# Optimization experiments

Measured on AMD Instinct MI355X. Metric: run time of the kernel, lower is better.

## Reference

```python
import jax, jax.numpy as jnp
import numpy as np

N_NODES = 30000
N_EDGES = 480000
NODE_DIM = 16
NUM_RADIAL = 8
NUM_ELEMENTS = 120
R_MAX = 5.0
NUM_BLOCKS = 2
N_PATHS = 5  # h0*sh0->0e, h0*sh1->1o, h0*sh2->2e, h1.sh1->0e, h2.sh2->0e


def _sh_basis(u):
    # real spherical harmonics up to l=2, component normalization, on unit vectors u [E,3]
    x, y, z = u[:, 0], u[:, 1], u[:, 2]
    s15 = jnp.sqrt(jnp.asarray(15.0, u.dtype))
    s5 = jnp.sqrt(jnp.asarray(5.0, u.dtype))
    sh1 = jnp.sqrt(jnp.asarray(3.0, u.dtype)) * u                      # [E,3]
    sh2 = jnp.stack([s15 * x * y, s15 * y * z,
                     0.5 * s5 * (3.0 * z * z - 1.0),
                     s15 * x * z, 0.5 * s15 * (x * x - y * y)], -1)    # [E,5]
    return sh1, sh2


def _energy(pos, emb, W_init, Wr, br, W_out, W_read, W1, b1, W2, b2, z, edge_index):
    N = pos.shape[0]
    row, col = edge_index[0], edge_index[1]
    edge_vec = pos[row] - pos[col]                                     # [E,3] gather
    r = jnp.sqrt(jnp.sum(edge_vec * edge_vec, -1) + 1e-12)             # [E]
    n = jnp.arange(1, NUM_RADIAL + 1, dtype=pos.dtype)
    # Bessel radial basis: sqrt(2/rc) * sin(n*pi*r/rc)/r
    radial = jnp.sqrt(2.0 / R_MAX) * jnp.sin(n[None, :] * jnp.pi * r[:, None] / R_MAX) / r[:, None]  # [E,R]
    u = edge_vec / r[:, None]
    sh1, sh2 = _sh_basis(u)

    # initial projection: embedding scalars -> 0e channels; l=1,l=2 start at zero
    h0 = emb[z] @ W_init                                               # [N,C]
    h1 = jnp.zeros((N, NODE_DIM, 3), pos.dtype)
    h2 = jnp.zeros((N, NODE_DIM, 5), pos.dtype)

    for b in range(NUM_BLOCKS):
        w = (radial @ Wr[b] + br[b]).reshape(-1, N_PATHS, NODE_DIM)    # [E,P,C] radial path weights
        h0c, h1c, h2c = h0[col], h1[col], h2[col]
        # scalar messages: h0*sh0 + <h1,sh1> + <h2,sh2>
        m0 = (w[:, 0] * h0c
              + w[:, 3] * jnp.einsum('ecm,em->ec', h1c, sh1)
              + w[:, 4] * jnp.einsum('ecm,em->ec', h2c, sh2))          # [E,C]
        m1 = (w[:, 1] * h0c)[:, :, None] * sh1[:, None, :]             # [E,C,3]
        m2 = (w[:, 2] * h0c)[:, :, None] * sh2[:, None, :]             # [E,C,5]
        a0 = jax.ops.segment_sum(m0, row, num_segments=N)
        a1 = jax.ops.segment_sum(m1, row, num_segments=N)
        a2 = jax.ops.segment_sum(m2, row, num_segments=N)
        h0 = h0 + a0 @ W_out[b, 0]
        h1 = h1 + jnp.einsum('ncm,cd->ndm', a1, W_out[b, 1])
        h2 = h2 + jnp.einsum('ncm,cd->ndm', a2, W_out[b, 2])

    inv = h0 @ W_read                                                  # readout 0e part
    site = jax.nn.silu(inv @ W1 + b1) @ W2 + b2                        # [N,1]
    return jnp.sum(site)


def setup_inputs() -> dict:
    key = jax.random.key(0)
    ks = jax.random.split(key, 12)
    C, R = NODE_DIM, NUM_RADIAL
    s = 1.0 / np.sqrt(C)
    return {
        'pos': jax.random.normal(ks[0], (N_NODES, 3), jnp.float32) * 3.0,
        'z': jax.random.randint(ks[1], (N_NODES,), 0, NUM_ELEMENTS),
        'edge_index': jax.random.randint(ks[2], (2, N_EDGES), 0, N_NODES),
        'emb': jax.random.normal(ks[3], (NUM_ELEMENTS, C), jnp.float32),
        'W_init': jax.random.normal(ks[4], (C, C), jnp.float32) * s,
        'Wr': jax.random.normal(ks[5], (NUM_BLOCKS, R, N_PATHS * C), jnp.float32) / np.sqrt(R),
        'br': jnp.zeros((NUM_BLOCKS, N_PATHS * C), jnp.float32),
        'W_out': jax.random.normal(ks[6], (NUM_BLOCKS, 3, C, C), jnp.float32) * s,
        'W_read': jax.random.normal(ks[7], (C, C), jnp.float32) * s,
        'W1': jax.random.normal(ks[8], (C, C), jnp.float32) * s,
        'b1': jnp.zeros((C,), jnp.float32),
        'W2': jax.random.normal(ks[9], (C, 1), jnp.float32) * s,
        'b2': jnp.zeros((1,), jnp.float32),
    }


def reference(pos, z, edge_index, emb, W_init, Wr, br, W_out, W_read, W1, b1, W2, b2):
    e_fn = lambda p: _energy(p, emb, W_init, Wr, br, W_out, W_read, W1, b1, W2, b2, z, edge_index)
    total, dE_dpos = jax.value_and_grad(e_fn)(pos)
    energy = jnp.reshape(total, (1, 1))
    forces = -dE_dpos
    return energy, forces
```

## Files before the change

### kernel.cpp

```cpp
#include <hip/hip_runtime.h>
#include <math.h>

#ifndef M_PI
#define M_PI 3.14159265358979323846
#endif

static inline int cdiv(int a, int b){ return (a + b - 1) / b; }

#define SQRT3f  1.7320508075688772f
#define SQRT5f  2.23606797749979f
#define SQRT15f 3.872983346207417f
#define KRADf   0.6324555320336759f
#define PI5f    0.6283185307179586f

__device__ __forceinline__ float grp16_sum(float v){
  v += __shfl_xor(v, 1, 64);
  v += __shfl_xor(v, 2, 64);
  v += __shfl_xor(v, 4, 64);
  v += __shfl_xor(v, 8, 64);
  return v;
}

__device__ __forceinline__ void sh_from_u(float ux, float uy, float uz,
                                          float* sh1, float* sh2)
{
  sh1[0] = SQRT3f*ux; sh1[1] = SQRT3f*uy; sh1[2] = SQRT3f*uz;
  sh2[0] = SQRT15f*ux*uy;
  sh2[1] = SQRT15f*uy*uz;
  sh2[2] = 0.5f*SQRT5f*(3.f*uz*uz - 1.f);
  sh2[3] = SQRT15f*ux*uz;
  sh2[4] = 0.5f*SQRT15f*(ux*ux - uy*uy);
}

__global__ void k_hist(const int* __restrict__ ei, int E,
                       int* __restrict__ deg_row, int* __restrict__ deg_col)
{
  int e = blockIdx.x * blockDim.x + threadIdx.x;
  if (e >= E) return;
  atomicAdd(&deg_row[ei[e]], 1);
  atomicAdd(&deg_col[ei[E + e]], 1);
}

__global__ void k_alloc(const int* __restrict__ deg_row, const int* __restrict__ deg_col,
                        int* __restrict__ start_row, int* __restrict__ cur_row,
                        int* __restrict__ start_col, int* __restrict__ cur_col,
                        int* __restrict__ cursors, int N)
{
  int idx = blockIdx.x * blockDim.x + threadIdx.x;
  int lane = threadIdx.x & 63;
  #pragma unroll
  for (int which = 0; which < 2; which++) {
    const int* deg = which ? deg_col : deg_row;
    int* start = which ? start_col : start_row;
    int* cur   = which ? cur_col   : cur_row;
    int v = (idx < N) ? deg[idx] : 0;
    int incl = v;
    #pragma unroll
    for (int d = 1; d < 64; d <<= 1) {
      int y = __shfl_up(incl, d, 64);
      if (lane >= d) incl += y;
    }
    int wtot = __shfl(incl, 63, 64);
    int base = 0;
    if (lane == 63) base = atomicAdd(&cursors[which], wtot);
    base = __shfl(base, 63, 64);
    if (idx < N) { int st = base + incl - v; start[idx] = st; cur[idx] = st; }
  }
}

__global__ void k_scatter_geom(const float* __restrict__ pos, const int* __restrict__ ei, int E,
                               int* __restrict__ cur_row, int* __restrict__ cur_col,
                               float4* __restrict__ geoR,
                               int* __restrict__ colR, int* __restrict__ cposR,
                               int* __restrict__ rowC, int* __restrict__ rposC)
{
  int e = blockIdx.x * blockDim.x + threadIdx.x;
  if (e >= E) return;
  int row = ei[e], col = ei[E + e];
  int pr = atomicAdd(&cur_row[row], 1);
  int pc = atomicAdd(&cur_col[col], 1);
  colR[pr] = col; cposR[pr] = pc;
  rowC[pc] = row; rposC[pc] = pr;

  float px = pos[row*3+0] - pos[col*3+0];
  float py = pos[row*3+1] - pos[col*3+1];
  float pz = pos[row*3+2] - pos[col*3+2];
  float r2 = px*px + py*py + pz*pz + 1e-12f;
  float r = sqrtf(r2);
  float inv_r = 1.0f / r;
  float ux = px*inv_r, uy = py*inv_r, uz = pz*inv_r;
  float x = r * PI5f;
  float s1, c1;
  sincosf(x, &s1, &c1);
  float tc = 2.f * c1;
  float sprev = 0.f, s = s1, cprev = 1.f, cc = c1;
  float Ki = KRADf * inv_r;
  float rad[8], draddr[8];
  const float KPI5 = KRADf * PI5f;
  #pragma unroll
  for (int k = 0; k < 8; k++) {
    rad[k] = Ki * s;
    draddr[k] = (KPI5 * (float)(k+1) * cc - rad[k]) * inv_r;
    float sn = tc*s - sprev; sprev = s; s = sn;
    float cn = tc*cc - cprev; cprev = cc; cc = cn;
  }
  geoR[pr*5+0] = make_float4(rad[0], rad[1], rad[2], rad[3]);
  geoR[pr*5+1] = make_float4(rad[4], rad[5], rad[6], rad[7]);
  geoR[pr*5+2] = make_float4(draddr[0], draddr[1], draddr[2], draddr[3]);
  geoR[pr*5+3] = make_float4(draddr[4], draddr[5], draddr[6], draddr[7]);
  geoR[pr*5+4] = make_float4(ux, uy, uz, inv_r);
}

__global__ void k_node_init(const float* __restrict__ emb, const int* __restrict__ z,
                            const float* __restrict__ W_init, float* __restrict__ h0, int N)
{
  __shared__ float sW[256];
  if (threadIdx.x < 256) sW[threadIdx.x] = W_init[threadIdx.x];
  __syncthreads();
  int n = blockIdx.x * blockDim.x + threadIdx.x;
  if (n >= N) return;
  const float* e = emb + z[n]*16;
  float ev[16];
  #pragma unroll
  for (int k = 0; k < 16; k++) ev[k] = e[k];
  #pragma unroll
  for (int c = 0; c < 16; c++) {
    float s = 0.f;
    #pragma unroll
    for (int k = 0; k < 16; k++) s += ev[k] * sW[k*16+c];
    h0[n*16+c] = s;
  }
}

__global__ void k_fwd_b0(const float* __restrict__ Wr, const float* __restrict__ br,
                         const float* __restrict__ h0_in, const float4* __restrict__ geoR,
                         const int* __restrict__ colR,
                         const int* __restrict__ start_row, const int* __restrict__ deg_row,
                         float* __restrict__ a0, float* __restrict__ a1, float* __restrict__ a2,
                         int N)
{
  int n = blockIdx.x * (blockDim.x >> 4) + (threadIdx.x >> 4);
  int c = threadIdx.x & 15;
  if (n >= N) return;
  float wr0[8], wr1[8], wr2[8];
  #pragma unroll
  for (int k = 0; k < 8; k++) {
    wr0[k] = Wr[k*80 + c];
    wr1[k] = Wr[k*80 + 16 + c];
    wr2[k] = Wr[k*80 + 32 + c];
  }
  float b0v = br[c], b1v = br[16 + c], b2v = br[32 + c];

  float acc0 = 0.f, acc1[3] = {0.f,0.f,0.f}, acc2[5] = {0.f,0.f,0.f,0.f,0.f};

  int i0 = start_row[n], i1 = i0 + deg_row[n];
  float4 G0n = {0,0,0,0}, G1n = {0,0,0,0}, G4n = {0,0,0,0};
  float h0n = 0.f;
  if (i0 < i1) {
    G0n = geoR[i0*5+0]; G1n = geoR[i0*5+1]; G4n = geoR[i0*5+4];
    h0n = h0_in[colR[i0]*16 + c];
  }
  for (int i = i0; i < i1; i++) {
    float4 G0 = G0n, G1 = G1n, G4 = G4n;
    float h0c = h0n;
    if (i+1 < i1) {
      G0n = geoR[(i+1)*5+0]; G1n = geoR[(i+1)*5+1]; G4n = geoR[(i+1)*5+4];
      h0n = h0_in[colR[i+1]*16 + c];
    }
    float rad[8] = {G0.x,G0.y,G0.z,G0.w,G1.x,G1.y,G1.z,G1.w};
    float sh1[3], sh2[5];
    sh_from_u(G4.x, G4.y, G4.z, sh1, sh2);
    float w0 = b0v, w1 = b1v, w2 = b2v;
    #pragma unroll
    for (int k = 0; k < 8; k++) {
      w0 += rad[k]*wr0[k]; w1 += rad[k]*wr1[k]; w2 += rad[k]*wr2[k];
    }
    acc0 += w0*h0c;
    float wh1 = w1*h0c, wh2 = w2*h0c;
    #pragma unroll
    for (int m = 0; m < 3; m++) acc1[m] += wh1*sh1[m];
    #pragma unroll
    for (int m = 0; m < 5; m++) acc2[m] += wh2*sh2[m];
  }
  a0[n*16 + c] = acc0;
  #pragma unroll
  for (int m = 0; m < 3; m++) a1[n*48 + c*3 + m] = acc1[m];
  #pragma unroll
  for (int m = 0; m < 5; m++) a2[n*80 + c*5 + m] = acc2[m];
}

__global__ void k_fwd_b1(const float* __restrict__ Wr, const float* __restrict__ br,
                         const float* __restrict__ h0_in, const float* __restrict__ h1_in,
                         const float* __restrict__ h2_in, const float4* __restrict__ geoR,
                         const int* __restrict__ colR,
                         const int* __restrict__ start_row, const int* __restrict__ deg_row,
                         float* __restrict__ a0, int N)
{
  int n = blockIdx.x * (blockDim.x >> 4) + (threadIdx.x >> 4);
  int c = threadIdx.x & 15;
  if (n >= N) return;
  float wr0[8], wr3[8], wr4[8];
  #pragma unroll
  for (int k = 0; k < 8; k++) {
    wr0[k] = Wr[k*80 + c];
    wr3[k] = Wr[k*80 + 48 + c];
    wr4[k] = Wr[k*80 + 64 + c];
  }
  float b0v = br[c], b3v = br[48 + c], b4v = br[64 + c];

  float acc0 = 0.f;
  int i0 = start_row[n], i1 = i0 + deg_row[n];
  float4 G0n = {0,0,0,0}, G1n = {0,0,0,0}, G4n = {0,0,0,0};
  float h0n = 0.f, h1n[3] = {0,0,0}, h2n[5] = {0,0,0,0,0};
  if (i0 < i1) {
    int col = colR[i0];
    G0n = geoR[i0*5+0]; G1n = geoR[i0*5+1]; G4n = geoR[i0*5+4];
    h0n = h0_in[col*16 + c];
    #pragma unroll
    for (int m = 0; m < 3; m++) h1n[m] = h1_in[col*48 + c*3 + m];
    #pragma unroll
    for (int m = 0; m < 5; m++) h2n[m] = h2_in[col*80 + c*5 + m];
  }
  for (int i = i0; i < i1; i++) {
    float4 G0 = G0n, G1 = G1n, G4 = G4n;
    float h0c = h0n;
    float h1c[3], h2c[5];
    #pragma unroll
    for (int m = 0; m < 3; m++) h1c[m] = h1n[m];
    #pragma unroll
    for (int m = 0; m < 5; m++) h2c[m] = h2n[m];
    if (i+1 < i1) {
      int col = colR[i+1];
      G0n = geoR[(i+1)*5+0]; G1n = geoR[(i+1)*5+1]; G4n = geoR[(i+1)*5+4];
      h0n = h0_in[col*16 + c];
      #pragma unroll
      for (int m = 0; m < 3; m++) h1n[m] = h1_in[col*48 + c*3 + m];
      #pragma unroll
      for (int m = 0; m < 5; m++) h2n[m] = h2_in[col*80 + c*5 + m];
    }
    float rad[8] = {G0.x,G0.y,G0.z,G0.w,G1.x,G1.y,G1.z,G1.w};
    float sh1[3], sh2[5];
    sh_from_u(G4.x, G4.y, G4.z, sh1, sh2);
    float w0 = b0v, w3 = b3v, w4 = b4v;
    #pragma unroll
    for (int k = 0; k < 8; k++) {
      w0 += rad[k]*wr0[k]; w3 += rad[k]*wr3[k]; w4 += rad[k]*wr4[k];
    }
    float S1 = 0.f, S2 = 0.f;
    #pragma unroll
    for (int m = 0; m < 3; m++) S1 += h1c[m]*sh1[m];
    #pragma unroll
    for (int m = 0; m < 5; m++) S2 += h2c[m]*sh2[m];
    acc0 += w0*h0c + w3*S1 + w4*S2;
  }
  a0[n*16 + c] = acc0;
}

__global__ void k_node_update(const float* __restrict__ h0_in,
                              const float* __restrict__ a0, const float* __restrict__ a1,
                              const float* __restrict__ a2,
                              const float* __restrict__ U,
                              float* __restrict__ h0_out, float* __restrict__ h1_out,
                              float* __restrict__ h2_out, int N, int full)
{
  int idx = blockIdx.x * blockDim.x + threadIdx.x;
  int n = idx >> 4, d = idx & 15;
  if (n >= N) return;
  const float* U0 = U;
  const float* U1 = U + 256;
  const float* U2 = U + 512;
  float s = h0_in[n*16 + d];
  #pragma unroll
  for (int c = 0; c < 16; c++) s += a0[n*16 + c] * U0[c*16 + d];
  h0_out[n*16 + d] = s;
  if (full) {
    float v1[3] = {0.f, 0.f, 0.f};
    #pragma unroll
    for (int c = 0; c < 16; c++) {
      float u = U1[c*16 + d];
      #pragma unroll
      for (int m = 0; m < 3; m++) v1[m] += a1[n*48 + c*3 + m] * u;
    }
    #pragma unroll
    for (int m = 0; m < 3; m++) h1_out[n*48 + d*3 + m] = v1[m];
    float v2[5] = {0.f, 0.f, 0.f, 0.f, 0.f};
    #pragma unroll
    for (int c = 0; c < 16; c++) {
      float u = U2[c*16 + d];
      #pragma unroll
      for (int m = 0; m < 5; m++) v2[m] += a2[n*80 + c*5 + m] * u;
    }
    #pragma unroll
    for (int m = 0; m < 5; m++) h2_out[n*80 + d*5 + m] = v2[m];
  }
}

__global__ void k_readout_bwd(const float* __restrict__ h0, const float* __restrict__ W_read,
                              const float* __restrict__ W1, const float* __restrict__ b1,
                              const float* __restrict__ W2, const float* __restrict__ b2,
                              float* __restrict__ g0, float* __restrict__ energy, int N)
{
  int n = blockIdx.x * blockDim.x + threadIdx.x;
  float site = 0.f;
  if (n < N) {
    float h[16], inv[16], dt[16];
    #pragma unroll
    for (int d = 0; d < 16; d++) h[d] = h0[n*16 + d];
    #pragma unroll
    for (int j = 0; j < 16; j++) {
      float s = 0.f;
      #pragma unroll
      for (int d = 0; d < 16; d++) s += h[d] * W_read[d*16 + j];
      inv[j] = s;
    }
    site = b2[0];
    #pragma unroll
    for (int c = 0; c < 16; c++) {
      float t = b1[c];
      #pragma unroll
      for (int j = 0; j < 16; j++) t += inv[j] * W1[j*16 + c];
      float sg = 1.f / (1.f + expf(-t));
      float w2v = W2[c];
      site += t * sg * w2v;
      dt[c] = w2v * sg * (1.f + t * (1.f - sg));
    }
    float dinv[16];
    #pragma unroll
    for (int j = 0; j < 16; j++) {
      float s = 0.f;
      #pragma unroll
      for (int c = 0; c < 16; c++) s += dt[c] * W1[j*16 + c];
      dinv[j] = s;
    }
    #pragma unroll
    for (int d = 0; d < 16; d++) {
      float s = 0.f;
      #pragma unroll
      for (int j = 0; j < 16; j++) s += dinv[j] * W_read[d*16 + j];
      g0[n*16 + d] = s;
    }
  }
  #pragma unroll
  for (int off = 32; off; off >>= 1) site += __shfl_down(site, off, 64);
  if ((threadIdx.x & 63) == 0) atomicAdd(energy, site);
}

__global__ void k_ga(const float* __restrict__ g0, const float* __restrict__ g1,
                     const float* __restrict__ g2, const float* __restrict__ U,
                     float* __restrict__ ga0, float* __restrict__ ga1, float* __restrict__ ga2,
                     int N, int full)
{
  int idx = blockIdx.x * blockDim.x + threadIdx.x;
  int n = idx >> 4, c = idx & 15;
  if (n >= N) return;
  const float* U0 = U;
  const float* U1 = U + 256;
  const float* U2 = U + 512;
  float s = 0.f;
  #pragma unroll
  for (int d = 0; d < 16; d++) s += g0[n*16 + d] * U0[c*16 + d];
  ga0[n*16 + c] = s;
  if (full) {
    float v1[3] = {0.f, 0.f, 0.f};
    #pragma unroll
    for (int d = 0; d < 16; d++) {
      float u = U1[c*16 + d];
      #pragma unroll
      for (int m = 0; m < 3; m++) v1[m] += g1[n*48 + d*3 + m] * u;
    }
    #pragma unroll
    for (int m = 0; m < 3; m++) ga1[n*48 + c*3 + m] = v1[m];
    float v2[5] = {0.f, 0.f, 0.f, 0.f, 0.f};
    #pragma unroll
    for (int d = 0; d < 16; d++) {
      float u = U2[c*16 + d];
      #pragma unroll
      for (int m = 0; m < 5; m++) v2[m] += g2[n*80 + d*5 + m] * u;
    }
    #pragma unroll
    for (int m = 0; m < 5; m++) ga2[n*80 + c*5 + m] = v2[m];
  }
}

__global__ void k_bwd_b1_col(const float* __restrict__ Wr, const float* __restrict__ br,
                             const float* __restrict__ h0_in, const float* __restrict__ h1_in,
                             const float* __restrict__ h2_in,
                             const float* __restrict__ ga0, const float4* __restrict__ geoR,
                             const int* __restrict__ rowC, const int* __restrict__ rposC,
                             const int* __restrict__ start_col, const int* __restrict__ deg_col,
                             float* __restrict__ g0, float* __restrict__ g1, float* __restrict__ g2,
                             float* __restrict__ dv_col, int N)
{
  int n = blockIdx.x * (blockDim.x >> 4) + (threadIdx.x >> 4);
  int c = threadIdx.x & 15;
  if (n >= N) return;
  float wr0[8], wr3[8], wr4[8];
  #pragma unroll
  for (int k = 0; k < 8; k++) {
    wr0[k] = Wr[k*80 + c];
    wr3[k] = Wr[k*80 + 48 + c];
    wr4[k] = Wr[k*80 + 64 + c];
  }
  float b0v = br[c], b3v = br[48 + c], b4v = br[64 + c];

  float h0c = h0_in[n*16 + c];
  float h1c[3], h2c[5];
  #pragma unroll
  for (int m = 0; m < 3; m++) h1c[m] = h1_in[n*48 + c*3 + m];
  #pragma unroll
  for (int m = 0; m < 5; m++) h2c[m] = h2_in[n*80 + c*5 + m];

  float accg0 = 0.f, accg1[3] = {0.f,0.f,0.f}, accg2[5] = {0.f,0.f,0.f,0.f,0.f};

  int i0 = start_col[n], i1 = i0 + deg_col[n];
  float4 G0n = {0,0,0,0}, G1n = {0,0,0,0}, G2n = {0,0,0,0}, G3n = {0,0,0,0}, G4n = {0,0,0,0};
  float dm0n = 0.f;
  if (i0 < i1) {
    int rp = rposC[i0];
    G0n = geoR[rp*5+0]; G1n = geoR[rp*5+1]; G2n = geoR[rp*5+2];
    G3n = geoR[rp*5+3]; G4n = geoR[rp*5+4];
    dm0n = ga0[rowC[i0]*16 + c];
  }
  for (int i = i0; i < i1; i++) {
    float4 G0 = G0n, G1 = G1n, G2 = G2n, G3 = G3n, G4 = G4n;
    float dm0 = dm0n;
    if (i+1 < i1) {
      int rp = rposC[i+1];
      G0n = geoR[rp*5+0]; G1n = geoR[rp*5+1]; G2n = geoR[rp*5+2];
      G3n = geoR[rp*5+3]; G4n = geoR[rp*5+4];
      dm0n = ga0[rowC[i+1]*16 + c];
    }
    float rad[8]    = {G0.x,G0.y,G0.z,G0.w,G1.x,G1.y,G1.z,G1.w};
    float draddr[8] = {G2.x,G2.y,G2.z,G2.w,G3.x,G3.y,G3.z,G3.w};
    float ux = G4.x, uy = G4.y, uz = G4.z, inv_r = G4.w;
    float sh1[3], sh2[5];
    sh_from_u(ux, uy, uz, sh1, sh2);

    float w0 = b0v, w3 = b3v, w4 = b4v;
    #pragma unroll
    for (int k = 0; k < 8; k++) {
      w0 += rad[k]*wr0[k]; w3 += rad[k]*wr3[k]; w4 += rad[k]*wr4[k];
    }

    float S1 = 0.f, S2 = 0.f;
    #pragma unroll
    for (int m = 0; m < 3; m++) S1 += h1c[m]*sh1[m];
    #pragma unroll
    for (int m = 0; m < 5; m++) S2 += h2c[m]*sh2[m];

    float dw0 = dm0 * h0c;
    float dw3 = dm0 * S1;
    float dw4 = dm0 * S2;
    float t3 = dm0 * w3, t4 = dm0 * w4;

    accg0 += dm0 * w0;
    #pragma unroll
    for (int m = 0; m < 3; m++) accg1[m] += t3 * sh1[m];
    #pragma unroll
    for (int m = 0; m < 5; m++) accg2[m] += t4 * sh2[m];

    float q1x = t3*h1c[0], q1y = t3*h1c[1], q1z = t3*h1c[2];
    float q0 = t4*h2c[0], q1 = t4*h2c[1], q2 = t4*h2c[2], q3 = t4*h2c[3], q4 = t4*h2c[4];
    float gr = 0.f;
    #pragma unroll
    for (int k = 0; k < 8; k++)
      gr += (dw0*wr0[k] + dw3*wr3[k] + dw4*wr4[k]) * draddr[k];
    float gux = SQRT3f*q1x + SQRT15f*(uy*q0 + uz*q3 + ux*q4);
    float guy = SQRT3f*q1y + SQRT15f*(ux*q0 + uz*q1 - uy*q4);
    float guz = SQRT3f*q1z + SQRT15f*uy*q1 + 3.f*SQRT5f*uz*q2 + SQRT15f*ux*q3;

    gr  = grp16_sum(gr);
    gux = grp16_sum(gux);
    guy = grp16_sum(guy);
    guz = grp16_sum(guz);

    if (c == 0) {
      float gdotu = gux*ux + guy*uy + guz*uz;
      dv_col[i*3+0] = gr*ux + (gux - gdotu*ux)*inv_r;
      dv_col[i*3+1] = gr*uy + (guy - gdotu*uy)*inv_r;
      dv_col[i*3+2] = gr*uz + (guz - gdotu*uz)*inv_r;
    }
  }
  g0[n*16 + c] += accg0;
  #pragma unroll
  for (int m = 0; m < 3; m++) g1[n*48 + c*3 + m] = accg1[m];
  #pragma unroll
  for (int m = 0; m < 5; m++) g2[n*80 + c*5 + m] = accg2[m];
}

__global__ void k_bwd_b0_row(const float* __restrict__ Wr, const float* __restrict__ br,
                             const float* __restrict__ h0_in,
                             const float* __restrict__ ga0, const float* __restrict__ ga1,
                             const float* __restrict__ ga2, const float4* __restrict__ geoR,
                             const int* __restrict__ colR, const int* __restrict__ cposR,
                             const int* __restrict__ start_row, const int* __restrict__ deg_row,
                             float* __restrict__ dv_col, int N)
{
  int n = blockIdx.x * (blockDim.x >> 4) + (threadIdx.x >> 4);
  int c = threadIdx.x & 15;
  if (n >= N) return;
  float wr0[8], wr1[8], wr2[8];
  #pragma unroll
  for (int k = 0; k < 8; k++) {
    wr0[k] = Wr[k*80 + c];
    wr1[k] = Wr[k*80 + 16 + c];
    wr2[k] = Wr[k*80 + 32 + c];
  }
  float b1v = br[16 + c], b2v = br[32 + c];

  float dm0 = ga0[n*16 + c];
  float dm1[3], dm2[5];
  #pragma unroll
  for (int m = 0; m < 3; m++) dm1[m] = ga1[n*48 + c*3 + m];
  #pragma unroll
  for (int m = 0; m < 5; m++) dm2[m] = ga2[n*80 + c*5 + m];

  int i0 = start_row[n], i1 = i0 + deg_row[n];
  float4 G0n = {0,0,0,0}, G1n = {0,0,0,0}, G2n = {0,0,0,0}, G3n = {0,0,0,0}, G4n = {0,0,0,0};
  float h0n = 0.f;
  if (i0 < i1) {
    G0n = geoR[i0*5+0]; G1n = geoR[i0*5+1]; G2n = geoR[i0*5+2];
    G3n = geoR[i0*5+3]; G4n = geoR[i0*5+4];
    h0n = h0_in[colR[i0]*16 + c];
  }
  for (int i = i0; i < i1; i++) {
    float4 G0 = G0n, G1 = G1n, G2 = G2n, G3 = G3n, G4 = G4n;
    float h0c = h0n;
    if (i+1 < i1) {
      G0n = geoR[(i+1)*5+0]; G1n = geoR[(i+1)*5+1]; G2n = geoR[(i+1)*5+2];
      G3n = geoR[(i+1)*5+3]; G4n = geoR[(i+1)*5+4];
      h0n = h0_in[colR[i+1]*16 + c];
    }
    float rad[8]    = {G0.x,G0.y,G0.z,G0.w,G1.x,G1.y,G1.z,G1.w};
    float draddr[8] = {G2.x,G2.y,G2.z,G2.w,G3.x,G3.y,G3.z,G3.w};
    float ux = G4.x, uy = G4.y, uz = G4.z, inv_r = G4.w;
    float sh1[3], sh2[5];
    sh_from_u(ux, uy, uz, sh1, sh2);

    float w1 = b1v, w2v = b2v;
    #pragma unroll
    for (int k = 0; k < 8; k++) { w1 += rad[k]*wr1[k]; w2v += rad[k]*wr2[k]; }

    float T1 = 0.f, T2 = 0.f;
    #pragma unroll
    for (int m = 0; m < 3; m++) T1 += dm1[m]*sh1[m];
    #pragma unroll
    for (int m = 0; m < 5; m++) T2 += dm2[m]*sh2[m];

    float dw0 = dm0 * h0c;
    float dw1 = h0c * T1;
    float dw2 = h0c * T2;

    float w1h = w1*h0c, w2h = w2v*h0c;
    float q1x = dm1[0]*w1h, q1y = dm1[1]*w1h, q1z = dm1[2]*w1h;
    float q0 = dm2[0]*w2h, q1 = dm2[1]*w2h, q2 = dm2[2]*w2h, q3 = dm2[3]*w2h, q4 = dm2[4]*w2h;

    float gr = 0.f;
    #pragma unroll
    for (int k = 0; k < 8; k++)
      gr += (dw0*wr0[k] + dw1*wr1[k] + dw2*wr2[k]) * draddr[k];
    float gux = SQRT3f*q1x + SQRT15f*(uy*q0 + uz*q3 + ux*q4);
    float guy = SQRT3f*q1y + SQRT15f*(ux*q0 + uz*q1 - uy*q4);
    float guz = SQRT3f*q1z + SQRT15f*uy*q1 + 3.f*SQRT5f*uz*q2 + SQRT15f*ux*q3;

    gr  = grp16_sum(gr);
    gux = grp16_sum(gux);
    guy = grp16_sum(guy);
    guz = grp16_sum(guz);

    if (c == 0) {
      int cp = cposR[i];
      float gdotu = gux*ux + guy*uy + guz*uz;
      dv_col[cp*3+0] += gr*ux + (gux - gdotu*ux)*inv_r;
      dv_col[cp*3+1] += gr*uy + (guy - gdotu*uy)*inv_r;
      dv_col[cp*3+2] += gr*uz + (guz - gdotu*uz)*inv_r;
    }
  }
}

__global__ void k_force(const int* __restrict__ start_row, const int* __restrict__ deg_row,
                        const int* __restrict__ cposR,
                        const int* __restrict__ start_col, const int* __restrict__ deg_col,
                        const float* __restrict__ dv_col, float* __restrict__ force, int N)
{
  int n = blockIdx.x * blockDim.x + threadIdx.x;
  if (n >= N) return;
  float fx = 0.f, fy = 0.f, fz = 0.f;
  int c0 = start_col[n], c1 = c0 + deg_col[n];
  for (int i = c0; i < c1; i++) {
    fx += dv_col[i*3+0]; fy += dv_col[i*3+1]; fz += dv_col[i*3+2];
  }
  int r0 = start_row[n], r1 = r0 + deg_row[n];
  for (int i = r0; i < r1; i++) {
    int cp = cposR[i];
    fx -= dv_col[cp*3+0]; fy -= dv_col[cp*3+1]; fz -= dv_col[cp*3+2];
  }
  force[n*3+0] = fx; force[n*3+1] = fy; force[n*3+2] = fz;
}

extern "C" void kernel_launch(void* const* d_in, const int* in_sizes, int n_in,
                              void* d_out, int out_size, void* d_ws, size_t ws_size,
                              hipStream_t stream)
{
  const float* pos    = (const float*)d_in[0];
  const int*   z      = (const int*)  d_in[1];
  const int*   ei     = (const int*)  d_in[2];
  const float* emb    = (const float*)d_in[3];
  const float* W_init = (const float*)d_in[4];
  const float* Wr     = (const float*)d_in[5];
  const float* br     = (const float*)d_in[6];
  const float* W_out  = (const float*)d_in[7];
  const float* W_read = (const float*)d_in[8];
  const float* W1     = (const float*)d_in[9];
  const float* b1     = (const float*)d_in[10];
  const float* W2     = (const float*)d_in[11];
  const float* b2     = (const float*)d_in[12];

  const int N = in_sizes[0] / 3;
  const int E = in_sizes[2] / 2;

  float* f = (float*)d_ws;
  float* geo_f = f; f += (size_t)E*20;
  float* h0_s0 = f; f += (size_t)N*16;
  float* h0_s1 = f; f += (size_t)N*16;
  float* h0_s2 = f; f += (size_t)N*16;
  float* h1_s1 = f; f += (size_t)N*48;
  float* h2_s1 = f; f += (size_t)N*80;
  float* a0    = f; f += (size_t)N*16;
  float* a1    = f; f += (size_t)N*48;
  float* a2    = f; f += (size_t)N*80;
  float* g0    = f; f += (size_t)N*16;
  float* g1    = f; f += (size_t)N*48;
  float* g2    = f; f += (size_t)N*80;
  float* dv    = f; f += (size_t)E*3;
  int* ip = (int*)f;
  int* cursors   = ip; ip += 2;
  int* deg_row   = ip; ip += N;
  int* deg_col   = ip; ip += N;
  int* start_row = ip; ip += N;
  int* start_col = ip; ip += N;
  int* cur_row   = ip; ip += N;
  int* cur_col   = ip; ip += N;
  int* colR      = ip; ip += E;
  int* cposR     = ip; ip += E;
  int* rowC      = ip; ip += E;
  int* rposC     = ip; ip += E;

  float4* geoR = (float4*)geo_f;

  float* out    = (float*)d_out;
  float* energy = out;
  float* force  = out + 1;

  const int BLK = 256;
  const int GPB = BLK / 16;

  (void)hipMemsetAsync(energy, 0, sizeof(float), stream);
  (void)hipMemsetAsync(cursors, 0, (size_t)(2 + 2*N) * sizeof(int), stream);

  k_hist<<<cdiv(E, BLK), BLK, 0, stream>>>(ei, E, deg_row, deg_col);
  k_alloc<<<cdiv(N, BLK), BLK, 0, stream>>>(deg_row, deg_col, start_row, cur_row,
                                            start_col, cur_col, cursors, N);
  k_scatter_geom<<<cdiv(E, BLK), BLK, 0, stream>>>(pos, ei, E, cur_row, cur_col,
                                                   geoR, colR, cposR, rowC, rposC);

  k_node_init<<<cdiv(N, BLK), BLK, 0, stream>>>(emb, z, W_init, h0_s0, N);

  k_fwd_b0<<<cdiv(N, GPB), BLK, 0, stream>>>(Wr, br, h0_s0, geoR, colR,
                                             start_row, deg_row, a0, a1, a2, N);
  k_node_update<<<cdiv(N*16, BLK), BLK, 0, stream>>>(h0_s0, a0, a1, a2,
                                                     W_out, h0_s1, h1_s1, h2_s1, N, 1);

  k_fwd_b1<<<cdiv(N, GPB), BLK, 0, stream>>>(Wr + 640, br + 80,
                                             h0_s1, h1_s1, h2_s1, geoR, colR,
                                             start_row, deg_row, a0, N);
  k_node_update<<<cdiv(N*16, BLK), BLK, 0, stream>>>(h0_s1, a0, nullptr, nullptr,
                                                     W_out + 768, h0_s2, nullptr, nullptr, N, 0);

  k_readout_bwd<<<cdiv(N, BLK), BLK, 0, stream>>>(h0_s2, W_read, W1, b1, W2, b2, g0, energy, N);

  k_ga<<<cdiv(N*16, BLK), BLK, 0, stream>>>(g0, nullptr, nullptr, W_out + 768,
                                            a0, nullptr, nullptr, N, 0);
  k_bwd_b1_col<<<cdiv(N, GPB), BLK, 0, stream>>>(Wr + 640, br + 80,
                                                 h0_s1, h1_s1, h2_s1, a0, geoR,
                                                 rowC, rposC, start_col, deg_col,
                                                 g0, g1, g2, dv, N);

  k_ga<<<cdiv(N*16, BLK), BLK, 0, stream>>>(g0, g1, g2, W_out, a0, a1, a2, N, 1);
  k_bwd_b0_row<<<cdiv(N, GPB), BLK, 0, stream>>>(Wr, br, h0_s0,
                                                 a0, a1, a2, geoR, colR, cposR,
                                                 start_row, deg_row, dv, N);

  k_force<<<cdiv(N, BLK), BLK, 0, stream>>>(start_row, deg_row, cposR,
                                            start_col, deg_col, dv, force, N);
}
```

Baseline: 555.7 us.

## Split each node's edge loop across four 16-lane groups and fuse first gradient projection

The four edge-processing kernels now give each node a full 64-lane wavefront, with four 16-lane groups taking interleaved edges and combining partial sums by cross-group shuffles. This raises parallelism and memory-level concurrency for nodes with many edges, which the serial per-node loop limited. The first k_ga launch is removed and its projection is folded into the readout kernel, saving one launch and a round trip of g0. The cost is extra shuffle reductions and lanes left idle on low-degree nodes.

```diff
diff --git a/kernel.cpp b/kernel.cpp
--- a/kernel.cpp
+++ b/kernel.cpp
@@ -18,6 +18,11 @@
   v += __shfl_xor(v, 2, 64);
   v += __shfl_xor(v, 4, 64);
   v += __shfl_xor(v, 8, 64);
+  return v;
+}
+__device__ __forceinline__ float xgrp_sum(float v){
+  v += __shfl_xor(v, 16, 64);
+  v += __shfl_xor(v, 32, 64);
   return v;
 }
 
@@ -139,8 +144,9 @@
                          float* __restrict__ a0, float* __restrict__ a1, float* __restrict__ a2,
                          int N)
 {
-  int n = blockIdx.x * (blockDim.x >> 4) + (threadIdx.x >> 4);
-  int c = threadIdx.x & 15;
+  int n = (blockIdx.x * blockDim.x + threadIdx.x) >> 6;
+  int lane = threadIdx.x & 63;
+  int g = lane >> 4, c = lane & 15;
   if (n >= N) return;
   float wr0[8], wr1[8], wr2[8];
   #pragma unroll
@@ -153,19 +159,19 @@
 
   float acc0 = 0.f, acc1[3] = {0.f,0.f,0.f}, acc2[5] = {0.f,0.f,0.f,0.f,0.f};
 
-  int i0 = start_row[n], i1 = i0 + deg_row[n];
+  int i0 = start_row[n] + g, i1 = start_row[n] + deg_row[n];
   float4 G0n = {0,0,0,0}, G1n = {0,0,0,0}, G4n = {0,0,0,0};
   float h0n = 0.f;
   if (i0 < i1) {
     G0n = geoR[i0*5+0]; G1n = geoR[i0*5+1]; G4n = geoR[i0*5+4];
     h0n = h0_in[colR[i0]*16 + c];
   }
-  for (int i = i0; i < i1; i++) {
+  for (int i = i0; i < i1; i += 4) {
     float4 G0 = G0n, G1 = G1n, G4 = G4n;
     float h0c = h0n;
-    if (i+1 < i1) {
-      G0n = geoR[(i+1)*5+0]; G1n = geoR[(i+1)*5+1]; G4n = geoR[(i+1)*5+4];
-      h0n = h0_in[colR[i+1]*16 + c];
+    if (i+4 < i1) {
+      G0n = geoR[(i+4)*5+0]; G1n = geoR[(i+4)*5+1]; G4n = geoR[(i+4)*5+4];
+      h0n = h0_in[colR[i+4]*16 + c];
     }
     float rad[8] = {G0.x,G0.y,G0.z,G0.w,G1.x,G1.y,G1.z,G1.w};
     float sh1[3], sh2[5];
@@ -182,11 +188,18 @@
     #pragma unroll
     for (int m = 0; m < 5; m++) acc2[m] += wh2*sh2[m];
   }
-  a0[n*16 + c] = acc0;
-  #pragma unroll
-  for (int m = 0; m < 3; m++) a1[n*48 + c*3 + m] = acc1[m];
-  #pragma unroll
-  for (int m = 0; m < 5; m++) a2[n*80 + c*5 + m] = acc2[m];
+  acc0 = xgrp_sum(acc0);
+  #pragma unroll
+  for (int m = 0; m < 3; m++) acc1[m] = xgrp_sum(acc1[m]);
+  #pragma unroll
+  for (int m = 0; m < 5; m++) acc2[m] = xgrp_sum(acc2[m]);
+  if (g == 0) {
+    a0[n*16 + c] = acc0;
+    #pragma unroll
+    for (int m = 0; m < 3; m++) a1[n*48 + c*3 + m] = acc1[m];
+    #pragma unroll
+    for (int m = 0; m < 5; m++) a2[n*80 + c*5 + m] = acc2[m];
+  }
 }
 
 __global__ void k_fwd_b1(const float* __restrict__ Wr, const float* __restrict__ br,
@@ -196,8 +209,9 @@
                          const int* __restrict__ start_row, const int* __restrict__ deg_row,
                          float* __restrict__ a0, int N)
 {
-  int n = blockIdx.x * (blockDim.x >> 4) + (threadIdx.x >> 4);
-  int c = threadIdx.x & 15;
+  int n = (blockIdx.x * blockDim.x + threadIdx.x) >> 6;
+  int lane = threadIdx.x & 63;
+  int g = lane >> 4, c = lane & 15;
   if (n >= N) return;
   float wr0[8], wr3[8], wr4[8];
   #pragma unroll
@@ -209,7 +223,7 @@
   float b0v = br[c], b3v = br[48 + c], b4v = br[64 + c];
 
   float acc0 = 0.f;
-  int i0 = start_row[n], i1 = i0 + deg_row[n];
+  int i0 = start_row[n] + g, i1 = start_row[n] + deg_row[n];
   float4 G0n = {0,0,0,0}, G1n = {0,0,0,0}, G4n = {0,0,0,0};
   float h0n = 0.f, h1n[3] = {0,0,0}, h2n[5] = {0,0,0,0,0};
   if (i0 < i1) {
@@ -221,7 +235,7 @@
     #pragma unroll
     for (int m = 0; m < 5; m++) h2n[m] = h2_in[col*80 + c*5 + m];
   }
-  for (int i = i0; i < i1; i++) {
+  for (int i = i0; i < i1; i += 4) {
     float4 G0 = G0n, G1 = G1n, G4 = G4n;
     float h0c = h0n;
     float h1c[3], h2c[5];
@@ -229,9 +243,9 @@
     for (int m = 0; m < 3; m++) h1c[m] = h1n[m];
     #pragma unroll
     for (int m = 0; m < 5; m++) h2c[m] = h2n[m];
-    if (i+1 < i1) {
-      int col = colR[i+1];
-      G0n = geoR[(i+1)*5+0]; G1n = geoR[(i+1)*5+1]; G4n = geoR[(i+1)*5+4];
+    if (i+4 < i1) {
+      int col = colR[i+4];
+      G0n = geoR[(i+4)*5+0]; G1n = geoR[(i+4)*5+1]; G4n = geoR[(i+4)*5+4];
       h0n = h0_in[col*16 + c];
       #pragma unroll
       for (int m = 0; m < 3; m++) h1n[m] = h1_in[col*48 + c*3 + m];
@@ -253,7 +267,8 @@
     for (int m = 0; m < 5; m++) S2 += h2c[m]*sh2[m];
     acc0 += w0*h0c + w3*S1 + w4*S2;
   }
-  a0[n*16 + c] = acc0;
+  acc0 = xgrp_sum(acc0);
+  if (g == 0) a0[n*16 + c] = acc0;
 }
 
 __global__ void k_node_update(const float* __restrict__ h0_in,
@@ -298,12 +313,14 @@
 __global__ void k_readout_bwd(const float* __restrict__ h0, const float* __restrict__ W_read,
                               const float* __restrict__ W1, const float* __restrict__ b1,
                               const float* __restrict__ W2, const float* __restrict__ b2,
-                              float* __restrict__ g0, float* __restrict__ energy, int N)
+                              const float* __restrict__ U0b1,
+                              float* __restrict__ g0, float* __restrict__ ga0,
+                              float* __restrict__ energy, int N)
 {
   int n = blockIdx.x * blockDim.x + threadIdx.x;
   float site = 0.f;
   if (n < N) {
-    float h[16], inv[16], dt[16];
+    float h[16], inv[16], dt[16], g0v[16];
     #pragma unroll
     for (int d = 0; d < 16; d++) h[d] = h0[n*16 + d];
     #pragma unroll
@@ -337,7 +354,15 @@
       float s = 0.f;
       #pragma unroll
       for (int j = 0; j < 16; j++) s += dinv[j] * W_read[d*16 + j];
+      g0v[d] = s;
       g0[n*16 + d] = s;
+    }
+    #pragma unroll
+    for (int c = 0; c < 16; c++) {
+      float s = 0.f;
+      #pragma unroll
+      for (int d = 0; d < 16; d++) s += g0v[d] * U0b1[c*16 + d];
+      ga0[n*16 + c] = s;
     }
   }
   #pragma unroll
@@ -348,7 +373,7 @@
 __global__ void k_ga(const float* __restrict__ g0, const float* __restrict__ g1,
                      const float* __restrict__ g2, const float* __restrict__ U,
                      float* __restrict__ ga0, float* __restrict__ ga1, float* __restrict__ ga2,
-                     int N, int full)
+                     int N)
 {
   int idx = blockIdx.x * blockDim.x + threadIdx.x;
   int n = idx >> 4, c = idx & 15;
@@ -360,26 +385,24 @@
   #pragma unroll
   for (int d = 0; d < 16; d++) s += g0[n*16 + d] * U0[c*16 + d];
   ga0[n*16 + c] = s;
-  if (full) {
-    float v1[3] = {0.f, 0.f, 0.f};
-    #pragma unroll
-    for (int d = 0; d < 16; d++) {
-      float u = U1[c*16 + d];
-      #pragma unroll
-      for (int m = 0; m < 3; m++) v1[m] += g1[n*48 + d*3 + m] * u;
-    }
-    #pragma unroll
-    for (int m = 0; m < 3; m++) ga1[n*48 + c*3 + m] = v1[m];
-    float v2[5] = {0.f, 0.f, 0.f, 0.f, 0.f};
-    #pragma unroll
-    for (int d = 0; d < 16; d++) {
-      float u = U2[c*16 + d];
-      #pragma unroll
-      for (int m = 0; m < 5; m++) v2[m] += g2[n*80 + d*5 + m] * u;
-    }
-    #pragma unroll
-    for (int m = 0; m < 5; m++) ga2[n*80 + c*5 + m] = v2[m];
-  }
+  float v1[3] = {0.f, 0.f, 0.f};
+  #pragma unroll
+  for (int d = 0; d < 16; d++) {
+    float u = U1[c*16 + d];
+    #pragma unroll
+    for (int m = 0; m < 3; m++) v1[m] += g1[n*48 + d*3 + m] * u;
+  }
+  #pragma unroll
+  for (int m = 0; m < 3; m++) ga1[n*48 + c*3 + m] = v1[m];
+  float v2[5] = {0.f, 0.f, 0.f, 0.f, 0.f};
+  #pragma unroll
+  for (int d = 0; d < 16; d++) {
+    float u = U2[c*16 + d];
+    #pragma unroll
+    for (int m = 0; m < 5; m++) v2[m] += g2[n*80 + d*5 + m] * u;
+  }
+  #pragma unroll
+  for (int m = 0; m < 5; m++) ga2[n*80 + c*5 + m] = v2[m];
 }
 
 __global__ void k_bwd_b1_col(const float* __restrict__ Wr, const float* __restrict__ br,
@@ -391,8 +414,9 @@
                              float* __restrict__ g0, float* __restrict__ g1, float* __restrict__ g2,
                              float* __restrict__ dv_col, int N)
 {
-  int n = blockIdx.x * (blockDim.x >> 4) + (threadIdx.x >> 4);
-  int c = threadIdx.x & 15;
+  int n = (blockIdx.x * blockDim.x + threadIdx.x) >> 6;
+  int lane = threadIdx.x & 63;
+  int g = lane >> 4, c = lane & 15;
   if (n >= N) return;
   float wr0[8], wr3[8], wr4[8];
   #pragma unroll
@@ -412,7 +436,7 @@
 
   float accg0 = 0.f, accg1[3] = {0.f,0.f,0.f}, accg2[5] = {0.f,0.f,0.f,0.f,0.f};
 
-  int i0 = start_col[n], i1 = i0 + deg_col[n];
+  int i0 = start_col[n] + g, i1 = start_col[n] + deg_col[n];
   float4 G0n = {0,0,0,0}, G1n = {0,0,0,0}, G2n = {0,0,0,0}, G3n = {0,0,0,0}, G4n = {0,0,0,0};
   float dm0n = 0.f;
   if (i0 < i1) {
@@ -421,14 +445,14 @@
     G3n = geoR[rp*5+3]; G4n = geoR[rp*5+4];
     dm0n = ga0[rowC[i0]*16 + c];
   }
-  for (int i = i0; i < i1; i++) {
+  for (int i = i0; i < i1; i += 4) {
     float4 G0 = G0n, G1 = G1n, G2 = G2n, G3 = G3n, G4 = G4n;
     float dm0 = dm0n;
-    if (i+1 < i1) {
-      int rp = rposC[i+1];
+    if (i+4 < i1) {
+      int rp = rposC[i+4];
       G0n = geoR[rp*5+0]; G1n = geoR[rp*5+1]; G2n = geoR[rp*5+2];
       G3n = geoR[rp*5+3]; G4n = geoR[rp*5+4];
-      dm0n = ga0[rowC[i+1]*16 + c];
+      dm0n = ga0[rowC[i+4]*16 + c];
     }
     float rad[8]    = {G0.x,G0.y,G0.z,G0.w,G1.x,G1.y,G1.z,G1.w};
     float draddr[8] = {G2.x,G2.y,G2.z,G2.w,G3.x,G3.y,G3.z,G3.w};
@@ -481,11 +505,18 @@
       dv_col[i*3+2] = gr*uz + (guz - gdotu*uz)*inv_r;
     }
   }
-  g0[n*16 + c] += accg0;
-  #pragma unroll
-  for (int m = 0; m < 3; m++) g1[n*48 + c*3 + m] = accg1[m];
-  #pragma unroll
-  for (int m = 0; m < 5; m++) g2[n*80 + c*5 + m] = accg2[m];
+  accg0 = xgrp_sum(accg0);
+  #pragma unroll
+  for (int m = 0; m < 3; m++) accg1[m] = xgrp_sum(accg1[m]);
+  #pragma unroll
+  for (int m = 0; m < 5; m++) accg2[m] = xgrp_sum(accg2[m]);
+  if (g == 0) {
+    g0[n*16 + c] += accg0;
+    #pragma unroll
+    for (int m = 0; m < 3; m++) g1[n*48 + c*3 + m] = accg1[m];
+    #pragma unroll
+    for (int m = 0; m < 5; m++) g2[n*80 + c*5 + m] = accg2[m];
+  }
 }
 
 __global__ void k_bwd_b0_row(const float* __restrict__ Wr, const float* __restrict__ br,
@@ -496,8 +527,9 @@
                              const int* __restrict__ start_row, const int* __restrict__ deg_row,
                              float* __restrict__ dv_col, int N)
 {
-  int n = blockIdx.x * (blockDim.x >> 4) + (threadIdx.x >> 4);
-  int c = threadIdx.x & 15;
+  int n = (blockIdx.x * blockDim.x + threadIdx.x) >> 6;
+  int lane = threadIdx.x & 63;
+  int g = lane >> 4, c = lane & 15;
   if (n >= N) return;
   float wr0[8], wr1[8], wr2[8];
   #pragma unroll
@@ -515,7 +547,7 @@
   #pragma unroll
   for (int m = 0; m < 5; m++) dm2[m] = ga2[n*80 + c*5 + m];
 
-  int i0 = start_row[n], i1 = i0 + deg_row[n];
+  int i0 = start_row[n] + g, i1 = start_row[n] + deg_row[n];
   float4 G0n = {0,0,0,0}, G1n = {0,0,0,0}, G2n = {0,0,0,0}, G3n = {0,0,0,0}, G4n = {0,0,0,0};
   float h0n = 0.f;
   if (i0 < i1) {
@@ -523,13 +555,13 @@
     G3n = geoR[i0*5+3]; G4n = geoR[i0*5+4];
     h0n = h0_in[colR[i0]*16 + c];
   }
-  for (int i = i0; i < i1; i++) {
+  for (int i = i0; i < i1; i += 4) {
     float4 G0 = G0n, G1 = G1n, G2 = G2n, G3 = G3n, G4 = G4n;
     float h0c = h0n;
-    if (i+1 < i1) {
-      G0n = geoR[(i+1)*5+0]; G1n = geoR[(i+1)*5+1]; G2n = geoR[(i+1)*5+2];
-      G3n = geoR[(i+1)*5+3]; G4n = geoR[(i+1)*5+4];
-      h0n = h0_in[colR[i+1]*16 + c];
+    if (i+4 < i1) {
+      G0n = geoR[(i+4)*5+0]; G1n = geoR[(i+4)*5+1]; G2n = geoR[(i+4)*5+2];
+      G3n = geoR[(i+4)*5+3]; G4n = geoR[(i+4)*5+4];
+      h0n = h0_in[colR[i+4]*16 + c];
     }
     float rad[8]    = {G0.x,G0.y,G0.z,G0.w,G1.x,G1.y,G1.z,G1.w};
     float draddr[8] = {G2.x,G2.y,G2.z,G2.w,G3.x,G3.y,G3.z,G3.w};
@@ -653,6 +685,7 @@
   float* force  = out + 1;
 
   const int BLK = 256;
+  const int NPB = BLK / 64;
   const int GPB = BLK / 16;
 
   (void)hipMemsetAsync(energy, 0, sizeof(float), stream);
@@ -666,28 +699,27 @@
 
   k_node_init<<<cdiv(N, BLK), BLK, 0, stream>>>(emb, z, W_init, h0_s0, N);
 
-  k_fwd_b0<<<cdiv(N, GPB), BLK, 0, stream>>>(Wr, br, h0_s0, geoR, colR,
+  k_fwd_b0<<<cdiv(N, NPB), BLK, 0, stream>>>(Wr, br, h0_s0, geoR, colR,
                                              start_row, deg_row, a0, a1, a2, N);
   k_node_update<<<cdiv(N*16, BLK), BLK, 0, stream>>>(h0_s0, a0, a1, a2,
                                                      W_out, h0_s1, h1_s1, h2_s1, N, 1);
 
-  k_fwd_b1<<<cdiv(N, GPB), BLK, 0, stream>>>(Wr + 640, br + 80,
+  k_fwd_b1<<<cdiv(N, NPB), BLK, 0, stream>>>(Wr + 640, br + 80,
                                              h0_s1, h1_s1, h2_s1, geoR, colR,
                                              start_row, deg_row, a0, N);
   k_node_update<<<cdiv(N*16, BLK), BLK, 0, stream>>>(h0_s1, a0, nullptr, nullptr,
                                                      W_out + 768, h0_s2, nullptr, nullptr, N, 0);
 
-  k_readout_bwd<<<cdiv(N, BLK), BLK, 0, stream>>>(h0_s2, W_read, W1, b1, W2, b2, g0, energy, N);
-
-  k_ga<<<cdiv(N*16, BLK), BLK, 0, stream>>>(g0, nullptr, nullptr, W_out + 768,
-                                            a0, nullptr, nullptr, N, 0);
-  k_bwd_b1_col<<<cdiv(N, GPB), BLK, 0, stream>>>(Wr + 640, br + 80,
+  k_readout_bwd<<<cdiv(N, BLK), BLK, 0, stream>>>(h0_s2, W_read, W1, b1, W2, b2,
+                                                  W_out + 768, g0, a0, energy, N);
+
+  k_bwd_b1_col<<<cdiv(N, NPB), BLK, 0, stream>>>(Wr + 640, br + 80,
                                                  h0_s1, h1_s1, h2_s1, a0, geoR,
                                                  rowC, rposC, start_col, deg_col,
                                                  g0, g1, g2, dv, N);
 
-  k_ga<<<cdiv(N*16, BLK), BLK, 0, stream>>>(g0, g1, g2, W_out, a0, a1, a2, N, 1);
-  k_bwd_b0_row<<<cdiv(N, GPB), BLK, 0, stream>>>(Wr, br, h0_s0,
+  k_ga<<<cdiv(N*16, BLK), BLK, 0, stream>>>(g0, g1, g2, W_out, a0, a1, a2, N);
+  k_bwd_b0_row<<<cdiv(N, NPB), BLK, 0, stream>>>(Wr, br, h0_s0,
                                                  a0, a1, a2, geoR, colR, cposR,
                                                  start_row, deg_row, dv, N);
 
```

Result: faster. 529.3 us (-4.7%).
